# Optimization experiments

Hardware: AMD Instinct MI355X
Metric: run time of the kernel (lower is better)

Reference implementation:

```python
import jax, jax.numpy as jnp
import numpy as np

B, IN, D, E, K = 16384, 2048, 1024, 3, 2
H1, H2 = 1024, 512


def setup_inputs() -> dict:
    key = jax.random.key(0)
    ks = jax.random.split(key, 10)
    x = jax.random.normal(ks[0], (B, IN), dtype=jnp.float32)
    gate = jax.random.normal(ks[1], (B, E), dtype=jnp.float32)
    topk_probs = jax.random.uniform(ks[2], (B, K), dtype=jnp.float32)
    topk_idx = jax.random.randint(ks[3], (B, K), 0, E)
    s = 0.02
    W1 = jax.random.normal(ks[4], (E, IN, H1), dtype=jnp.float32) * s
    b1 = jnp.zeros((E, H1), dtype=jnp.float32)
    W2 = jax.random.normal(ks[5], (E, H1, H2), dtype=jnp.float32) * s
    b2 = jnp.zeros((E, H2), dtype=jnp.float32)
    W3 = jax.random.normal(ks[6], (E, H2, D), dtype=jnp.float32) * s
    b3 = jnp.zeros((E, D), dtype=jnp.float32)
    return {"x": x, "gate": gate, "topk_probs": topk_probs, "topk_idx": topk_idx,
            "W1": W1, "b1": b1, "W2": W2, "b2": b2, "W3": W3, "b3": b3}


def _lrelu(v):
    return jnp.where(v > 0, v, 0.2 * v)  # LeakyReLU(0.2)


def reference(x, gate, topk_probs, topk_idx, W1, b1, W2, b2, W3, b3):
    # gate is accepted by the original forward but never used.
    n_experts = W1.shape[0]
    # Per-expert 3-layer MLP, batched over experts: [E, B, *]
    h = _lrelu(jnp.einsum('bi,eio->ebo', x, W1) + b1[:, None, :])
    h = _lrelu(jnp.einsum('ebi,eio->ebo', h, W2) + b2[:, None, :])
    y = jnp.einsum('ebi,eio->ebo', h, W3) + b3[:, None, :]  # [E, B, D]
    # Combine: weight for expert e on token b = sum_k probs[b,k] * [idx[b,k]==e]
    onehot = topk_idx[None, :, :] == jnp.arange(n_experts)[:, None, None]  # [E,B,K]
    w = jnp.sum(jnp.where(onehot, topk_probs[None, :, :], 0.0), axis=-1)  # [E,B]
    return jnp.einsum('eb,ebd->bd', w, y)
```

## Files before the change

### kernel.cpp

```cpp
#include <hip/hip_runtime.h>
#include <cstdint>
#include <cstddef>

#define B_TOK   16384
#define IN_DIM  2048
#define D_DIM   1024
#define NEXP    3
#define TOPK    2
#define H1_DIM  1024
#define H2_DIM  512

typedef __bf16 bf16x8 __attribute__((ext_vector_type(8)));
typedef float  f32x4  __attribute__((ext_vector_type(4)));
typedef unsigned short ushort8_t __attribute__((ext_vector_type(8)));

__device__ __forceinline__ unsigned short f2bf(float f) {
    unsigned int u = __builtin_bit_cast(unsigned int, f);
    return (unsigned short)((u + 0x7fffu + ((u >> 16) & 1u)) >> 16);
}

__device__ __forceinline__ void glds16(const void* gsrc, void* ldst) {
    __builtin_amdgcn_global_load_lds(
        (__attribute__((address_space(1))) void*)(gsrc),
        (__attribute__((address_space(3))) void*)(ldst),
        16, 0, 0);
}


__global__ __launch_bounds__(256) void convert_f32_bf16(
    const float* __restrict__ in, unsigned short* __restrict__ out, size_t n)
{
    size_t i = ((size_t)blockIdx.x * blockDim.x + threadIdx.x) * 8;
    size_t stride = (size_t)gridDim.x * blockDim.x * 8;
    for (; i < n; i += stride) {
        float4 a = *(const float4*)(in + i);
        float4 b = *(const float4*)(in + i + 4);
        ushort8_t o;
        o[0] = f2bf(a.x); o[1] = f2bf(a.y); o[2] = f2bf(a.z); o[3] = f2bf(a.w);
        o[4] = f2bf(b.x); o[5] = f2bf(b.y); o[6] = f2bf(b.z); o[7] = f2bf(b.w);
        *(ushort8_t*)(out + i) = o;
    }
}

__global__ __launch_bounds__(256) void transpose_convert(
    const float* __restrict__ W, unsigned short* __restrict__ Wt, int K, int N)
{
    __shared__ unsigned short tile[64][68];
    int e = blockIdx.z;
    const float* Wp = W + (size_t)e * K * N;
    unsigned short* Wtp = Wt + (size_t)e * N * K;
    int n0 = blockIdx.x * 64, k0 = blockIdx.y * 64;
    int t = threadIdx.x;
    int nn = (t & 15) * 4;
    int kk = t >> 4;
    #pragma unroll
    for (int r = 0; r < 4; ++r) {
        int k = kk + r * 16;
        float4 v = *(const float4*)(Wp + (size_t)(k0 + k) * N + (n0 + nn));
        tile[k][nn + 0] = f2bf(v.x);
        tile[k][nn + 1] = f2bf(v.y);
        tile[k][nn + 2] = f2bf(v.z);
        tile[k][nn + 3] = f2bf(v.w);
    }
    __syncthreads();
    int n  = t >> 2;
    int kb = (t & 3) * 16;
    ushort8_t o0, o1;
    #pragma unroll
    for (int i = 0; i < 8; ++i) o0[i] = tile[kb + i][n];
    #pragma unroll
    for (int i = 0; i < 8; ++i) o1[i] = tile[kb + 8 + i][n];
    unsigned short* dst = Wtp + (size_t)(n0 + n) * K + (k0 + kb);
    *(ushort8_t*)dst = o0;
    *(ushort8_t*)(dst + 8) = o1;
}

__global__ __launch_bounds__(256) void route_tokens(
    const float* __restrict__ probs, const int* __restrict__ idx,
    int* __restrict__ cnt, int* __restrict__ list, float* __restrict__ wl)
{
    __shared__ int lcnt[NEXP];
    __shared__ int lbase[NEXP];
    __shared__ int ltok[NEXP][256];
    __shared__ float lww[NEXP][256];
    int t = threadIdx.x;
    int b = blockIdx.x * 256 + t;
    if (t < NEXP) lcnt[t] = 0;
    __syncthreads();
    float p0 = probs[b * TOPK + 0], p1 = probs[b * TOPK + 1];
    int   i0 = idx[b * TOPK + 0],   i1 = idx[b * TOPK + 1];
    #pragma unroll
    for (int e = 0; e < NEXP; ++e) {
        bool m0 = (i0 == e), m1 = (i1 == e);
        if (m0 || m1) {
            float w = (m0 ? p0 : 0.f) + (m1 ? p1 : 0.f);
            int s = atomicAdd(&lcnt[e], 1);
            ltok[e][s] = b; lww[e][s] = w;
        }
    }
    __syncthreads();
    if (t < NEXP) lbase[t] = atomicAdd(&cnt[t], lcnt[t]);
    __syncthreads();
    #pragma unroll
    for (int e = 0; e < NEXP; ++e) {
        int n = lcnt[e], base = lbase[e];
        for (int s = t; s < n; s += 256) {
            list[e * B_TOK + base + s] = ltok[e][s];
            wl[e * B_TOK + base + s]   = lww[e][s];
        }
    }
}

__global__ void finalize_counts(const int* __restrict__ cnt, int* __restrict__ cntp,
                                int* __restrict__ list, float* __restrict__ wl)
{
    int e = blockIdx.x;
    int c = cnt[e];
    int cp = (c + 255) & ~255;
    if (threadIdx.x == 0) cntp[e] = cp;
    for (int s = c + threadIdx.x; s < cp; s += blockDim.x) {
        list[e * B_TOK + s] = 0;
        wl[e * B_TOK + s] = 0.f;
    }
}

template<int ACT, int FINAL, int GATHER>
__global__ __launch_bounds__(512, 2) void gemm8(
    const unsigned short* __restrict__ Ab, size_t Aplane,
    const unsigned short* __restrict__ Bb,
    const float* __restrict__ biasb,
    unsigned short* __restrict__ Hb, size_t Hplane,
    float* __restrict__ outb,
    const float* __restrict__ wlb,
    const int* __restrict__ listb,
    const int* __restrict__ cnt,
    const int* __restrict__ cntp,
    int N, int K, int NT, int e0)
{
    const int bid  = blockIdx.x;
    const int xcd  = bid & 7;
    const int slot = bid >> 3;
    const int q    = slot / NT;
    const int nt   = slot % NT;
    const int ti   = q * 8 + xcd;
    const int e    = e0 + (ti >> 6);
    const int mt   = ti & 63;
    const int bm   = mt << 8;
    if (bm >= cntp[e]) return;
    const int bn   = nt << 8;

    __shared__ char smem[131072];

    const int tid  = threadIdx.x;
    const int lane = tid & 63;
    const int w    = tid >> 6;
    const int wl3  = w & 3;
    const int wn1  = w >> 2;
    const int l15  = lane & 15;
    const int ug8  = (((tid & 7) ^ ((tid >> 3) & 7)) << 3);
    const int sw0  = ((((lane >> 4) + 0) ^ (lane & 7)) << 4);
    const int sw1  = ((((lane >> 4) + 4) ^ (lane & 7)) << 4);

    const int* listp = listb + (size_t)e * B_TOK;
    const unsigned short* Ae = Ab + (size_t)e * Aplane;
    const unsigned short* Be = Bb + (size_t)e * ((size_t)N * K);
    const float* biasp = biasb + (size_t)e * N;

    const unsigned short* sA[2][2];
    const unsigned short* sB[2][2];
    #pragma unroll
    for (int h = 0; h < 2; ++h)
        #pragma unroll
        for (int j = 0; j < 2; ++j) {
            int lrow = h * 128 + j * 64 + (tid >> 3);
            int arow;
            if constexpr (GATHER) arow = listp[bm + lrow];
            else                  arow = bm + lrow;
            sA[h][j] = Ae + (size_t)arow * K + ug8;
            sB[h][j] = Be + (size_t)(bn + lrow) * K + ug8;
        }

    char* const stA = smem + (w << 10);
    char* const stB = smem + 65536 + (w << 10);
    const char* const rA = smem + (wl3 * 32 + l15) * 128;
    const char* const rB = smem + 65536 + (wn1 * 64 + l15) * 128;

    f32x4 acc[2][2][2][4] = {};
    bf16x8 av[2][2];
    bf16x8 bv[4][2];

#define STA(db, h, kt) do {                                                     \
    glds16(sA[h][0] + (size_t)(kt) * 64, stA + (db) * 32768 + (h) * 16384);     \
    glds16(sA[h][1] + (size_t)(kt) * 64, stA + (db) * 32768 + (h) * 16384 + 8192); } while (0)
#define STB(db, h, kt) do {                                                     \
    glds16(sB[h][0] + (size_t)(kt) * 64, stB + (db) * 32768 + (h) * 16384);     \
    glds16(sB[h][1] + (size_t)(kt) * 64, stB + (db) * 32768 + (h) * 16384 + 8192); } while (0)

#define LA(db, Qm) do {                                                         \
    _Pragma("unroll")                                                           \
    for (int ml = 0; ml < 2; ++ml) {                                            \
        av[ml][0] = *(const bf16x8*)(rA + (db)*32768 + (Qm)*16384 + ml*2048 + sw0); \
        av[ml][1] = *(const bf16x8*)(rA + (db)*32768 + (Qm)*16384 + ml*2048 + sw1); \
    } } while (0)
#define LB(db, Qn) do {                                                         \
    _Pragma("unroll")                                                           \
    for (int nl = 0; nl < 4; ++nl) {                                            \
        bv[nl][0] = *(const bf16x8*)(rB + (db)*32768 + (Qn)*16384 + nl*2048 + sw0); \
        bv[nl][1] = *(const bf16x8*)(rB + (db)*32768 + (Qn)*16384 + nl*2048 + sw1); \
    } } while (0)

#define WINDOW(Qm, Qn, STAGE_STMT, VM_STMT, NEXT_LOADS) do {                    \
    STAGE_STMT;                                                                 \
    asm volatile("s_waitcnt lgkmcnt(0)" ::: "memory");                          \
    __builtin_amdgcn_sched_barrier(0);                                          \
    __builtin_amdgcn_s_setprio(1);                                              \
    _Pragma("unroll")                                                           \
    for (int ml = 0; ml < 2; ++ml)                                              \
        _Pragma("unroll")                                                       \
        for (int nl = 0; nl < 4; ++nl) {                                        \
            acc[Qm][ml][Qn][nl] = __builtin_amdgcn_mfma_f32_16x16x32_bf16(      \
                av[ml][0], bv[nl][0], acc[Qm][ml][Qn][nl], 0, 0, 0);            \
            acc[Qm][ml][Qn][nl] = __builtin_amdgcn_mfma_f32_16x16x32_bf16(      \
                av[ml][1], bv[nl][1], acc[Qm][ml][Qn][nl], 0, 0, 0);            \
        }                                                                       \
    __builtin_amdgcn_s_setprio(0);                                              \
    VM_STMT;                                                                    \
    NEXT_LOADS;                                                                 \
    __builtin_amdgcn_sched_barrier(0);                                          \
    __builtin_amdgcn_s_barrier();                                               \
} while (0)

    const int nkt = K >> 6;
    STA(0, 0, 0); STA(0, 1, 0); STB(0, 0, 0); STB(0, 1, 0);
    STA(1, 0, 1); STB(1, 0, 1);
    asm volatile("s_waitcnt vmcnt(4)" ::: "memory");
    __builtin_amdgcn_s_barrier();
    LA(0, 1); LB(0, 0);

    const int niter = nkt >> 1;
    for (int it = 0; it < niter; ++it) {
        const int t1 = 2 * it + 1;
        const int t2 = (2 * it + 2 < nkt) ? 2 * it + 2 : nkt - 1;
        const int t3 = (2 * it + 3 < nkt) ? 2 * it + 3 : nkt - 1;
        WINDOW(1, 0, STA(1, 1, t1), ((void)0), LA(0, 0));
        WINDOW(0, 0, STB(1, 1, t1), ((void)0), LB(0, 1));
        WINDOW(0, 1, STA(0, 0, t2), ((void)0), LA(0, 1));
        WINDOW(1, 1, STB(0, 0, t2),
               asm volatile("s_waitcnt vmcnt(4)" ::: "memory"), LA(1, 1); LB(1, 0));
        WINDOW(1, 0, STA(0, 1, t2), ((void)0), LA(1, 0));
        WINDOW(0, 0, STB(0, 1, t2), ((void)0), LB(1, 1));
        WINDOW(0, 1, STA(1, 0, t3), ((void)0), LA(1, 1));
        WINDOW(1, 1, STB(1, 0, t3),
               asm volatile("s_waitcnt vmcnt(4)" ::: "memory"), LA(0, 1); LB(0, 0));
    }
    asm volatile("s_waitcnt vmcnt(0)" ::: "memory");

    const int rl = (lane >> 4) << 2;
    float bsv[2][4];
    #pragma unroll
    for (int Qn = 0; Qn < 2; ++Qn)
        #pragma unroll
        for (int nl = 0; nl < 4; ++nl)
            bsv[Qn][nl] = biasp[bn + Qn * 128 + wn1 * 64 + nl * 16 + l15];

    if constexpr (!FINAL) {
        unsigned short* Hp = Hb + (size_t)e * Hplane;
        #pragma unroll
        for (int Qm = 0; Qm < 2; ++Qm)
        #pragma unroll
        for (int ml = 0; ml < 2; ++ml)
        #pragma unroll
        for (int jj = 0; jj < 4; ++jj) {
            int srow = bm + Qm * 128 + wl3 * 32 + ml * 16 + rl + jj;
            size_t ro = (size_t)srow * N;
            #pragma unroll
            for (int Qn = 0; Qn < 2; ++Qn)
            #pragma unroll
            for (int nl = 0; nl < 4; ++nl) {
                int col = bn + Qn * 128 + wn1 * 64 + nl * 16 + l15;
                float v = acc[Qm][ml][Qn][nl][jj] + bsv[Qn][nl];
                if (ACT) v = v > 0.f ? v : 0.2f * v;
                Hp[ro + col] = f2bf(v);
            }
        }
    } else {
        const int C = cnt[e];
        const float* wlp = wlb + (size_t)e * B_TOK;
        #pragma unroll
        for (int Qm = 0; Qm < 2; ++Qm)
        #pragma unroll
        for (int ml = 0; ml < 2; ++ml)
        #pragma unroll
        for (int jj = 0; jj < 4; ++jj) {
            int srow = bm + Qm * 128 + wl3 * 32 + ml * 16 + rl + jj;
            if (srow < C) {
                int tok = listp[srow];
                float wv = wlp[srow];
                size_t ro = (size_t)tok * D_DIM;
                #pragma unroll
                for (int Qn = 0; Qn < 2; ++Qn)
                #pragma unroll
                for (int nl = 0; nl < 4; ++nl) {
                    int col = bn + Qn * 128 + wn1 * 64 + nl * 16 + l15;
                    atomicAdd(&outb[ro + col],
                              (acc[Qm][ml][Qn][nl][jj] + bsv[Qn][nl]) * wv);
                }
            }
        }
    }
#undef WINDOW
#undef LA
#undef LB
#undef STA
#undef STB
}


extern "C" void kernel_launch(void* const* d_in, const int* in_sizes, int n_in,
                              void* d_out, int out_size, void* d_ws, size_t ws_size,
                              hipStream_t stream)
{
    const float* x     = (const float*)d_in[0];
    const float* probs = (const float*)d_in[2];
    const int*   tidx  = (const int*)d_in[3];
    const float* W1    = (const float*)d_in[4];
    const float* b1    = (const float*)d_in[5];
    const float* W2    = (const float*)d_in[6];
    const float* b2    = (const float*)d_in[7];
    const float* W3    = (const float*)d_in[8];
    const float* b3    = (const float*)d_in[9];
    float* out = (float*)d_out;

    char* ws = (char*)d_ws;
    const size_t xb_off  = 0;
    const size_t w1t_off = xb_off  + (size_t)B_TOK * IN_DIM * 2;
    const size_t w2t_off = w1t_off + (size_t)NEXP * IN_DIM * H1_DIM * 2;
    const size_t w3t_off = w2t_off + (size_t)NEXP * H1_DIM * H2_DIM * 2;
    const size_t h1_off  = w3t_off + (size_t)NEXP * H2_DIM * D_DIM * 2;
    const size_t h2_off  = h1_off  + (size_t)NEXP * B_TOK * H1_DIM * 2;
    const size_t li_off  = h2_off  + (size_t)NEXP * B_TOK * H2_DIM * 2;
    const size_t wl_off  = li_off  + (size_t)NEXP * B_TOK * 4;
    const size_t cn_off  = wl_off  + (size_t)NEXP * B_TOK * 4;
    const size_t cp_off  = cn_off  + 256;

    unsigned short* xb  = (unsigned short*)(ws + xb_off);
    unsigned short* W1t = (unsigned short*)(ws + w1t_off);
    unsigned short* W2t = (unsigned short*)(ws + w2t_off);
    unsigned short* W3t = (unsigned short*)(ws + w3t_off);
    unsigned short* h1  = (unsigned short*)(ws + h1_off);
    unsigned short* h2  = (unsigned short*)(ws + h2_off);
    int*            lst = (int*)(ws + li_off);
    float*          wl  = (float*)(ws + wl_off);
    int*            cnt = (int*)(ws + cn_off);
    int*            cnp = (int*)(ws + cp_off);

    hipMemsetAsync(out, 0, (size_t)out_size * sizeof(float), stream);
    hipMemsetAsync(cnt, 0, 256, stream);

    convert_f32_bf16<<<2048, 256, 0, stream>>>(x, xb, (size_t)B_TOK * IN_DIM);
    transpose_convert<<<dim3(H1_DIM / 64, IN_DIM / 64, NEXP), 256, 0, stream>>>(W1, W1t, IN_DIM, H1_DIM);
    transpose_convert<<<dim3(H2_DIM / 64, H1_DIM / 64, NEXP), 256, 0, stream>>>(W2, W2t, H1_DIM, H2_DIM);
    transpose_convert<<<dim3(D_DIM / 64, H2_DIM / 64, NEXP), 256, 0, stream>>>(W3, W3t, H2_DIM, D_DIM);
    route_tokens<<<B_TOK / 256, 256, 0, stream>>>(probs, tidx, cnt, lst, wl);
    finalize_counts<<<NEXP, 256, 0, stream>>>(cnt, cnp, lst, wl);

    const size_t h1pl = (size_t)B_TOK * H1_DIM;
    const size_t h2pl = (size_t)B_TOK * H2_DIM;

    gemm8<1, 0, 1><<<dim3(NEXP * 64 * 4), 512, 0, stream>>>(
        xb, 0, W1t, b1, h1, h1pl, nullptr, nullptr,
        lst, cnt, cnp, H1_DIM, IN_DIM, 4, 0);
    gemm8<1, 0, 0><<<dim3(NEXP * 64 * 2), 512, 0, stream>>>(
        h1, h1pl, W2t, b2, h2, h2pl, nullptr, nullptr,
        lst, cnt, cnp, H2_DIM, H1_DIM, 2, 0);
    gemm8<0, 1, 0><<<dim3(NEXP * 64 * 4), 512, 0, stream>>>(
        h2, h2pl, W3t, b3, nullptr, 0, out, wl,
        lst, cnt, cnp, D_DIM, H2_DIM, 4, 0);
}
```

Measured before the change: 338.9 us.

## Replace atomic scatter-combine with per-expert Y buffer and gather combine kernel

The final GEMM now writes bias-added fp32 outputs into a per-expert Y buffer using plain stores instead of atomically adding weighted rows into the output. A new combine kernel looks up each token's row through an inverse index built during routing and computes p0*y0 + p1*y1. This also drops the output memset and the per-row weight list. Separately, the explicit lgkmcnt(0) wait in the MFMA window is removed and a scheduling barrier is added, leaving the compiler to insert the LDS waits. The trade-off is a large extra fp32 intermediate that must be written and read back, in exchange for avoiding float atomics.

```diff
diff --git a/kernel.cpp b/kernel.cpp
--- a/kernel.cpp
+++ b/kernel.cpp
@@ -77,25 +77,21 @@
 
 __global__ __launch_bounds__(256) void route_tokens(
     const float* __restrict__ probs, const int* __restrict__ idx,
-    int* __restrict__ cnt, int* __restrict__ list, float* __restrict__ wl)
+    int* __restrict__ cnt, int* __restrict__ list, int* __restrict__ inv)
 {
     __shared__ int lcnt[NEXP];
     __shared__ int lbase[NEXP];
     __shared__ int ltok[NEXP][256];
-    __shared__ float lww[NEXP][256];
     int t = threadIdx.x;
     int b = blockIdx.x * 256 + t;
     if (t < NEXP) lcnt[t] = 0;
     __syncthreads();
-    float p0 = probs[b * TOPK + 0], p1 = probs[b * TOPK + 1];
-    int   i0 = idx[b * TOPK + 0],   i1 = idx[b * TOPK + 1];
+    int i0 = idx[b * TOPK + 0], i1 = idx[b * TOPK + 1];
     #pragma unroll
     for (int e = 0; e < NEXP; ++e) {
-        bool m0 = (i0 == e), m1 = (i1 == e);
-        if (m0 || m1) {
-            float w = (m0 ? p0 : 0.f) + (m1 ? p1 : 0.f);
+        if (i0 == e || i1 == e) {
             int s = atomicAdd(&lcnt[e], 1);
-            ltok[e][s] = b; lww[e][s] = w;
+            ltok[e][s] = b;
         }
     }
     __syncthreads();
@@ -105,35 +101,57 @@
     for (int e = 0; e < NEXP; ++e) {
         int n = lcnt[e], base = lbase[e];
         for (int s = t; s < n; s += 256) {
-            list[e * B_TOK + base + s] = ltok[e][s];
-            wl[e * B_TOK + base + s]   = lww[e][s];
+            int tk = ltok[e][s];
+            list[e * B_TOK + base + s] = tk;
+            inv[e * B_TOK + tk] = base + s;
         }
     }
 }
 
 __global__ void finalize_counts(const int* __restrict__ cnt, int* __restrict__ cntp,
-                                int* __restrict__ list, float* __restrict__ wl)
+                                int* __restrict__ list)
 {
     int e = blockIdx.x;
     int c = cnt[e];
     int cp = (c + 255) & ~255;
     if (threadIdx.x == 0) cntp[e] = cp;
-    for (int s = c + threadIdx.x; s < cp; s += blockDim.x) {
+    for (int s = c + threadIdx.x; s < cp; s += blockDim.x)
         list[e * B_TOK + s] = 0;
-        wl[e * B_TOK + s] = 0.f;
-    }
-}
-
-template<int ACT, int FINAL, int GATHER>
+}
+
+__global__ __launch_bounds__(256) void combine_out(
+    const float* __restrict__ probs, const int* __restrict__ tidx,
+    const int* __restrict__ inv, const float* __restrict__ y, size_t ypl,
+    float* __restrict__ out)
+{
+    int gid = blockIdx.x * 256 + threadIdx.x;
+    int tok = gid >> 7;
+    int dc  = (gid & 127) << 3;
+    float p0 = probs[tok * TOPK + 0], p1 = probs[tok * TOPK + 1];
+    int   i0 = tidx [tok * TOPK + 0], i1 = tidx [tok * TOPK + 1];
+    size_t r0 = (size_t)i0 * ypl + (size_t)inv[(size_t)i0 * B_TOK + tok] * D_DIM + dc;
+    size_t r1 = (size_t)i1 * ypl + (size_t)inv[(size_t)i1 * B_TOK + tok] * D_DIM + dc;
+    float4 a0 = *(const float4*)(y + r0), a1 = *(const float4*)(y + r0 + 4);
+    float4 b0 = *(const float4*)(y + r1), b1 = *(const float4*)(y + r1 + 4);
+    float4 o0, o1;
+    o0.x = p0 * a0.x + p1 * b0.x;  o0.y = p0 * a0.y + p1 * b0.y;
+    o0.z = p0 * a0.z + p1 * b0.z;  o0.w = p0 * a0.w + p1 * b0.w;
+    o1.x = p0 * a1.x + p1 * b1.x;  o1.y = p0 * a1.y + p1 * b1.y;
+    o1.z = p0 * a1.z + p1 * b1.z;  o1.w = p0 * a1.w + p1 * b1.w;
+    float* op = out + (size_t)tok * D_DIM + dc;
+    *(float4*)op = o0;
+    *(float4*)(op + 4) = o1;
+}
+
+template<int ACT, int OUT32, int GATHER>
 __global__ __launch_bounds__(512, 2) void gemm8(
     const unsigned short* __restrict__ Ab, size_t Aplane,
     const unsigned short* __restrict__ Bb,
     const float* __restrict__ biasb,
-    unsigned short* __restrict__ Hb, size_t Hplane,
-    float* __restrict__ outb,
-    const float* __restrict__ wlb,
+    unsigned short* __restrict__ Hb,
+    float* __restrict__ Yb,
+    size_t plane,
     const int* __restrict__ listb,
-    const int* __restrict__ cnt,
     const int* __restrict__ cntp,
     int N, int K, int NT, int e0)
 {
@@ -211,7 +229,6 @@
 
 #define WINDOW(Qm, Qn, STAGE_STMT, VM_STMT, NEXT_LOADS) do {                    \
     STAGE_STMT;                                                                 \
-    asm volatile("s_waitcnt lgkmcnt(0)" ::: "memory");                          \
     __builtin_amdgcn_sched_barrier(0);                                          \
     __builtin_amdgcn_s_setprio(1);                                              \
     _Pragma("unroll")                                                           \
@@ -225,6 +242,7 @@
         }                                                                       \
     __builtin_amdgcn_s_setprio(0);                                              \
     VM_STMT;                                                                    \
+    __builtin_amdgcn_sched_barrier(0);                                          \
     NEXT_LOADS;                                                                 \
     __builtin_amdgcn_sched_barrier(0);                                          \
     __builtin_amdgcn_s_barrier();                                               \
@@ -263,8 +281,8 @@
         for (int nl = 0; nl < 4; ++nl)
             bsv[Qn][nl] = biasp[bn + Qn * 128 + wn1 * 64 + nl * 16 + l15];
 
-    if constexpr (!FINAL) {
-        unsigned short* Hp = Hb + (size_t)e * Hplane;
+    if constexpr (!OUT32) {
+        unsigned short* Hp = Hb + (size_t)e * plane;
         #pragma unroll
         for (int Qm = 0; Qm < 2; ++Qm)
         #pragma unroll
@@ -284,8 +302,7 @@
             }
         }
     } else {
-        const int C = cnt[e];
-        const float* wlp = wlb + (size_t)e * B_TOK;
+        float* Yp = Yb + (size_t)e * plane;
         #pragma unroll
         for (int Qm = 0; Qm < 2; ++Qm)
         #pragma unroll
@@ -293,18 +310,13 @@
         #pragma unroll
         for (int jj = 0; jj < 4; ++jj) {
             int srow = bm + Qm * 128 + wl3 * 32 + ml * 16 + rl + jj;
-            if (srow < C) {
-                int tok = listp[srow];
-                float wv = wlp[srow];
-                size_t ro = (size_t)tok * D_DIM;
-                #pragma unroll
-                for (int Qn = 0; Qn < 2; ++Qn)
-                #pragma unroll
-                for (int nl = 0; nl < 4; ++nl) {
-                    int col = bn + Qn * 128 + wn1 * 64 + nl * 16 + l15;
-                    atomicAdd(&outb[ro + col],
-                              (acc[Qm][ml][Qn][nl][jj] + bsv[Qn][nl]) * wv);
-                }
+            size_t ro = (size_t)srow * N;
+            #pragma unroll
+            for (int Qn = 0; Qn < 2; ++Qn)
+            #pragma unroll
+            for (int nl = 0; nl < 4; ++nl) {
+                int col = bn + Qn * 128 + wn1 * 64 + nl * 16 + l15;
+                Yp[ro + col] = acc[Qm][ml][Qn][nl][jj] + bsv[Qn][nl];
             }
         }
     }
@@ -338,9 +350,10 @@
     const size_t w3t_off = w2t_off + (size_t)NEXP * H1_DIM * H2_DIM * 2;
     const size_t h1_off  = w3t_off + (size_t)NEXP * H2_DIM * D_DIM * 2;
     const size_t h2_off  = h1_off  + (size_t)NEXP * B_TOK * H1_DIM * 2;
-    const size_t li_off  = h2_off  + (size_t)NEXP * B_TOK * H2_DIM * 2;
-    const size_t wl_off  = li_off  + (size_t)NEXP * B_TOK * 4;
-    const size_t cn_off  = wl_off  + (size_t)NEXP * B_TOK * 4;
+    const size_t y_off   = h2_off  + (size_t)NEXP * B_TOK * H2_DIM * 2;
+    const size_t li_off  = y_off   + (size_t)NEXP * B_TOK * D_DIM * 4;
+    const size_t iv_off  = li_off  + (size_t)NEXP * B_TOK * 4;
+    const size_t cn_off  = iv_off  + (size_t)NEXP * B_TOK * 4;
     const size_t cp_off  = cn_off  + 256;
 
     unsigned short* xb  = (unsigned short*)(ws + xb_off);
@@ -349,31 +362,34 @@
     unsigned short* W3t = (unsigned short*)(ws + w3t_off);
     unsigned short* h1  = (unsigned short*)(ws + h1_off);
     unsigned short* h2  = (unsigned short*)(ws + h2_off);
+    float*          y   = (float*)(ws + y_off);
     int*            lst = (int*)(ws + li_off);
-    float*          wl  = (float*)(ws + wl_off);
+    int*            inv = (int*)(ws + iv_off);
     int*            cnt = (int*)(ws + cn_off);
     int*            cnp = (int*)(ws + cp_off);
 
-    hipMemsetAsync(out, 0, (size_t)out_size * sizeof(float), stream);
     hipMemsetAsync(cnt, 0, 256, stream);
 
     convert_f32_bf16<<<2048, 256, 0, stream>>>(x, xb, (size_t)B_TOK * IN_DIM);
     transpose_convert<<<dim3(H1_DIM / 64, IN_DIM / 64, NEXP), 256, 0, stream>>>(W1, W1t, IN_DIM, H1_DIM);
     transpose_convert<<<dim3(H2_DIM / 64, H1_DIM / 64, NEXP), 256, 0, stream>>>(W2, W2t, H1_DIM, H2_DIM);
     transpose_convert<<<dim3(D_DIM / 64, H2_DIM / 64, NEXP), 256, 0, stream>>>(W3, W3t, H2_DIM, D_DIM);
-    route_tokens<<<B_TOK / 256, 256, 0, stream>>>(probs, tidx, cnt, lst, wl);
-    finalize_counts<<<NEXP, 256, 0, stream>>>(cnt, cnp, lst, wl);
+    route_tokens<<<B_TOK / 256, 256, 0, stream>>>(probs, tidx, cnt, lst, inv);
+    finalize_counts<<<NEXP, 256, 0, stream>>>(cnt, cnp, lst);
 
     const size_t h1pl = (size_t)B_TOK * H1_DIM;
     const size_t h2pl = (size_t)B_TOK * H2_DIM;
+    const size_t ypl  = (size_t)B_TOK * D_DIM;
 
     gemm8<1, 0, 1><<<dim3(NEXP * 64 * 4), 512, 0, stream>>>(
-        xb, 0, W1t, b1, h1, h1pl, nullptr, nullptr,
-        lst, cnt, cnp, H1_DIM, IN_DIM, 4, 0);
+        xb, 0, W1t, b1, h1, nullptr, h1pl,
+        lst, cnp, H1_DIM, IN_DIM, 4, 0);
     gemm8<1, 0, 0><<<dim3(NEXP * 64 * 2), 512, 0, stream>>>(
-        h1, h1pl, W2t, b2, h2, h2pl, nullptr, nullptr,
-        lst, cnt, cnp, H2_DIM, H1_DIM, 2, 0);
+        h1, h1pl, W2t, b2, h2, nullptr, h2pl,
+        lst, cnp, H2_DIM, H1_DIM, 2, 0);
     gemm8<0, 1, 0><<<dim3(NEXP * 64 * 4), 512, 0, stream>>>(
-        h2, h2pl, W3t, b3, nullptr, 0, out, wl,
-        lst, cnt, cnp, D_DIM, H2_DIM, 4, 0);
-}
+        h2, h2pl, W3t, b3, nullptr, y, ypl,
+        lst, cnp, D_DIM, H2_DIM, 4, 0);
+    combine_out<<<dim3(B_TOK * 128 / 256), 256, 0, stream>>>(
+        probs, tidx, inv, y, ypl, out);
+}
```

After: 302.7 us. 10.7% less time.
